# Kernel optimization log

Measured on AMD Instinct MI355X. Metric: run time of the kernel, lower is better.

Reference implementation:

```python
import jax, jax.numpy as jnp
import numpy as np

N = 100_000   # nodes
D = 64        # hidden = H * C
H, C = 8, 8   # heads, per-head channels
E = 500_000   # edges per edge set
EPS = 1e-3    # keras LayerNormalization default epsilon
RSQRT_C = np.float32(1.0 / np.sqrt(C))


def setup_inputs() -> dict:
    key = jax.random.key(0)
    ks = jax.random.split(key, 13)
    s = 0.05
    return dict(
        x=jax.random.normal(ks[0], (N, D), jnp.float32),
        src0=jax.random.randint(ks[1], (E,), 0, N, jnp.int32),
        dst0=jax.random.randint(ks[2], (E,), 0, N, jnp.int32),
        src1=jax.random.randint(ks[3], (E,), 0, N, jnp.int32),
        dst1=jax.random.randint(ks[4], (E,), 0, N, jnp.int32),
        Wk=jax.random.normal(ks[5], (D, D), jnp.float32) * s,
        bk=jnp.zeros((D,), jnp.float32),
        Wm=jax.random.normal(ks[6], (D, D), jnp.float32) * s,
        bm=jnp.zeros((D,), jnp.float32),
        Wq=jax.random.normal(ks[7], (D, D), jnp.float32) * s,
        bq=jnp.zeros((D,), jnp.float32),
        Wa=jax.random.normal(ks[8], (D, D), jnp.float32) * s,
        ba=jnp.zeros((D,), jnp.float32),
        Watt0=jax.random.normal(ks[9], (H, C, C), jnp.float32) * s,
        Wmsg0=jax.random.normal(ks[10], (H, C, C), jnp.float32) * s,
        prior0=jnp.ones((H,), jnp.float32),
        Watt1=jax.random.normal(ks[11], (H, C, C), jnp.float32) * s,
        Wmsg1=jax.random.normal(ks[12], (H, C, C), jnp.float32) * s,
        prior1=jnp.ones((H,), jnp.float32),
        skip_w=jnp.ones((1,), jnp.float32),
        ln_gamma=jnp.ones((D,), jnp.float32),
        ln_beta=jnp.zeros((D,), jnp.float32),
    )


def _edge_terms(k, m, q, src, dst, Watt, Wmsg, prior):
    # gather sender keys/messages, apply per-edge-set per-head projections
    ke = jnp.einsum('ehk,hkl->ehl', k[src], Watt)          # [E,H,C]
    score = jnp.einsum('ehc,ehc->eh', ke, q[dst]) * prior * RSQRT_C  # [E,H]
    me = jnp.einsum('ehk,hkl->ehl', m[src], Wmsg)          # [E,H,C]
    return score, me


def _forward(x, src0, dst0, src1, dst1, Wk, bk, Wm, bm, Wq, bq, Wa, ba,
             Watt0, Wmsg0, prior0, Watt1, Wmsg1, prior1,
             skip_w, ln_gamma, ln_beta):
    n = x.shape[0]
    split = lambda t: t.reshape(n, H, C)
    k = split(x @ Wk + bk)   # sender keys   [N,H,C]
    m = split(x @ Wm + bm)   # sender msgs   [N,H,C]
    q = split(x @ Wq + bq)   # receiver qrys [N,H,C]

    s0, m0 = _edge_terms(k, m, q, src0, dst0, Watt0, Wmsg0, prior0)
    s1, m1 = _edge_terms(k, m, q, src1, dst1, Watt1, Wmsg1, prior1)

    # joint segment softmax over ALL incoming edges per receiver (across edge sets)
    scores = jnp.concatenate([s0, s1], axis=0)  # [Et,H]
    msgs = jnp.concatenate([m0, m1], axis=0)    # [Et,H,C]
    recv = jnp.concatenate([dst0, dst1], axis=0)
    smax = jax.ops.segment_max(scores, recv, num_segments=n)
    ex = jnp.exp(scores - smax[recv])
    denom = jax.ops.segment_sum(ex, recv, num_segments=n)
    coef = ex / denom[recv]                      # [Et,H]

    pooled = jax.ops.segment_sum(coef[:, :, None] * msgs, recv, num_segments=n)  # [N,H,C]
    merged = pooled.reshape(n, D)
    agg = jax.nn.gelu(merged, approximate=False) @ Wa + ba
    # (dropout_rate=0.0 -> identity)
    sc = jax.nn.sigmoid(skip_w[0])               # learnable weighted skip
    out = sc * agg + (1.0 - sc) * x
    # layer norm (keras default eps=1e-3)
    mu = jnp.mean(out, axis=-1, keepdims=True)
    var = jnp.var(out, axis=-1, keepdims=True)
    return ln_gamma * (out - mu) * jax.lax.rsqrt(var + EPS) + ln_beta


def reference(x, src0, dst0, src1, dst1, Wk, bk, Wm, bm, Wq, bq, Wa, ba,
              Watt0, Wmsg0, prior0, Watt1, Wmsg1, prior1,
              skip_w, ln_gamma, ln_beta):
    return _forward(x, src0, dst0, src1, dst1, Wk, bk, Wm, bm, Wq, bq, Wa, ba,
                    Watt0, Wmsg0, prior0, Watt1, Wmsg1, prior1,
                    skip_w, ln_gamma, ln_beta)
```

## Files before the change

kernel.cpp:

```cpp
#include <hip/hip_runtime.h>
#include <hip/hip_fp16.h>
#include <cstdint>
#include <cstddef>

#define TPB 256
static constexpr float RSQRT_C_F = 0.35355339059327373f;

typedef __attribute__((ext_vector_type(8))) short bf16x8;
typedef __attribute__((ext_vector_type(4))) float f32x4;
typedef __attribute__((ext_vector_type(2))) float f32x2;

#if __has_builtin(__builtin_amdgcn_cvt_pk_f32_fp8) && __has_builtin(__builtin_amdgcn_cvt_pk_fp8_f32)
#define USE_HW_FP8 1
#endif

__device__ __forceinline__ unsigned short f2bf(float f) {
    unsigned u = __float_as_uint(f);
    u += 0x7FFFu + ((u >> 16) & 1u);
    return (unsigned short)(u >> 16);
}
__device__ __forceinline__ float bf2f(unsigned short h) {
    return __uint_as_float((unsigned)h << 16);
}
__device__ __forceinline__ float loF(unsigned u) { return __uint_as_float(u << 16); }
__device__ __forceinline__ float hiF(unsigned u) { return __uint_as_float(u); }

__device__ __forceinline__ unsigned char enc8(float v) {
#ifdef USE_HW_FP8
    return (unsigned char)(__builtin_amdgcn_cvt_pk_fp8_f32(v, v, 0, false) & 0xff);
#else
    unsigned s = (__float_as_uint(v) >> 24) & 0x80u;
    float a = fabsf(v);
    if (a < 0.015625f) {
        int m = __float2int_rn(a * 512.f);
        return (unsigned char)(s | (unsigned)m);
    }
    if (a > 448.f) return (unsigned char)(s | 0x7e);
    unsigned u = __float_as_uint(a);
    u += 0x7FFFFu + ((u >> 20) & 1u);
    unsigned e8 = ((u >> 23) & 0xffu) - 120u;
    unsigned m3 = (u >> 20) & 7u;
    if (e8 > 15u) return (unsigned char)(s | 0x7e);
    return (unsigned char)(s | (e8 << 3) | m3);
#endif
}

__device__ __forceinline__ void dec8x8(uint2 v, float* o) {
#ifdef USE_HW_FP8
    f32x2 a = __builtin_amdgcn_cvt_pk_f32_fp8((int)v.x, false);
    f32x2 b = __builtin_amdgcn_cvt_pk_f32_fp8((int)v.x, true);
    f32x2 c = __builtin_amdgcn_cvt_pk_f32_fp8((int)v.y, false);
    f32x2 d = __builtin_amdgcn_cvt_pk_f32_fp8((int)v.y, true);
    o[0] = a.x; o[1] = a.y; o[2] = b.x; o[3] = b.y;
    o[4] = c.x; o[5] = c.y; o[6] = d.x; o[7] = d.y;
#else
    unsigned w[2] = {v.x, v.y};
    #pragma unroll
    for (int i = 0; i < 8; i++) {
        unsigned bb = (w[i >> 2] >> ((i & 3) * 8)) & 0xffu;
        unsigned short hs = (unsigned short)(((bb & 0x80u) << 8) | ((bb & 0x7fu) << 7));
        __half h = *reinterpret_cast<__half*>(&hs);
        o[i] = 256.f * __half2float(h);
    }
#endif
}

__device__ __forceinline__ float wbig_elem(const float* __restrict__ Wq,
                                           const float* __restrict__ Wk,
                                           const float* __restrict__ Wm,
                                           const float* __restrict__ Watt0,
                                           const float* __restrict__ Watt1,
                                           const float* __restrict__ Wmsg0,
                                           const float* __restrict__ Wmsg1,
                                           const float* __restrict__ prior0,
                                           const float* __restrict__ prior1,
                                           int i, int col) {
    if (col < 64) return Wq[i * 64 + col];
    int j = col - 64, set = j >> 6, l = j & 63, h = l >> 3, lc = l & 7;
    const float* Win = (set < 2) ? Wk : Wm;
    const float* T = (set == 0) ? Watt0 : (set == 1) ? Watt1 : (set == 2) ? Wmsg0 : Wmsg1;
    float scale = (set == 0) ? prior0[h] * RSQRT_C_F
                : (set == 1) ? prior1[h] * RSQRT_C_F : 1.f;
    float acc = 0.f;
    #pragma unroll
    for (int c = 0; c < 8; c++) acc += Win[i * 64 + h * 8 + c] * T[h * 64 + c * 8 + lc];
    return acc * scale;
}

__global__ void setup_kernel(const float* __restrict__ Wq, const float* __restrict__ bq,
                             const float* __restrict__ Wk, const float* __restrict__ bk,
                             const float* __restrict__ Wm, const float* __restrict__ bm,
                             const float* __restrict__ Watt0, const float* __restrict__ prior0,
                             const float* __restrict__ Watt1, const float* __restrict__ prior1,
                             const float* __restrict__ Wmsg0, const float* __restrict__ Wmsg1,
                             const float* __restrict__ Wa,
                             float* __restrict__ bbig,
                             unsigned short* __restrict__ Wpack,
                             unsigned short* __restrict__ Wapack,
                             int4* __restrict__ subzero, int n4) {
    const int b = blockIdx.x, t = threadIdx.x;
    if (b < 12) {
        int p = b * TPB + t;
        if (p >= 48 * 64) return;
        bool isWa = (p >= 40 * 64);
        int pl = isWa ? p - 40 * 64 : p;
        int lane = pl & 63, ctkt = pl >> 6;
        int ct = ctkt >> 1, kt = ctkt & 1;
        int kbase = kt * 32 + (lane >> 4) * 8;
        int col = ct * 16 + (lane & 15);
        unsigned short h[8];
        if (isWa) {
            #pragma unroll
            for (int j = 0; j < 8; j++) h[j] = f2bf(Wa[(size_t)(kbase + j) * 64 + col]);
        } else {
            #pragma unroll
            for (int j = 0; j < 8; j++)
                h[j] = f2bf(wbig_elem(Wq, Wk, Wm, Watt0, Watt1, Wmsg0, Wmsg1,
                                      prior0, prior1, kbase + j, col));
        }
        uint4 pk;
        pk.x = (unsigned)h[0] | ((unsigned)h[1] << 16);
        pk.y = (unsigned)h[2] | ((unsigned)h[3] << 16);
        pk.z = (unsigned)h[4] | ((unsigned)h[5] << 16);
        pk.w = (unsigned)h[6] | ((unsigned)h[7] << 16);
        unsigned short* dst = isWa ? Wapack : Wpack;
        *(uint4*)&dst[(size_t)pl * 8] = pk;
    } else if (b < 14) {
        int col = (b - 12) * TPB + t;
        if (col >= 320) return;
        float v;
        if (col < 64) {
            v = bq[col];
        } else {
            int j = col - 64, set = j >> 6, l = j & 63, h = l >> 3, lc = l & 7;
            const float* bin = (set < 2) ? bk : bm;
            const float* T = (set == 0) ? Watt0 : (set == 1) ? Watt1 : (set == 2) ? Wmsg0 : Wmsg1;
            float scale = (set == 0) ? prior0[h] * RSQRT_C_F
                        : (set == 1) ? prior1[h] * RSQRT_C_F : 1.f;
            float acc = 0.f;
            #pragma unroll
            for (int c = 0; c < 8; c++) acc += bin[h * 8 + c] * T[h * 64 + c * 8 + lc];
            v = acc * scale;
        }
        bbig[col] = v;
    } else {
        int i = (b - 14) * TPB + t;
        int stride = 18 * TPB;
        for (; i < n4; i += stride) subzero[i] = int4{0, 0, 0, 0};
    }
}

__global__ void hist_kernel(const int* __restrict__ dst0, const int* __restrict__ dst1,
                            int* __restrict__ sub, int* __restrict__ rank,
                            int E0, int Etot, int N) {
    const int gid = blockIdx.x * TPB + threadIdx.x;
    const int S = gridDim.x * TPB;
    #pragma unroll
    for (int k = 0; k < 4; k++) {
        int e = gid + k * S;
        if (e < Etot) {
            int d = (e < E0) ? dst0[e] : dst1[e - E0];
            d = min(max(d, 0), N - 1);
            rank[e] = atomicAdd(&sub[((e >> 8) & 7) * N + d], 1);
        }
    }
}

__global__ void scan1(int* __restrict__ sub, int* __restrict__ offsets,
                      int* __restrict__ blocksums, int n) {
    __shared__ int sums[TPB];
    int b = blockIdx.x, t = threadIdx.x;
    int base = b * 1024 + t * 4;
    int cnt[4];
    #pragma unroll
    for (int i = 0; i < 4; i++) {
        int d = base + i;
        int s = 0;
        if (d < n) {
            #pragma unroll
            for (int bb = 0; bb < 8; bb++) {
                int v = sub[bb * n + d];
                sub[bb * n + d] = s;
                s += v;
            }
        }
        cnt[i] = s;
    }
    int local = cnt[0] + cnt[1] + cnt[2] + cnt[3];
    sums[t] = local;
    __syncthreads();
    for (int off = 1; off < TPB; off <<= 1) {
        int add = (t >= off) ? sums[t - off] : 0;
        __syncthreads();
        sums[t] += add;
        __syncthreads();
    }
    int excl = sums[t] - local;
    if (base + 0 < n) offsets[base + 0] = excl;
    if (base + 1 < n) offsets[base + 1] = excl + cnt[0];
    if (base + 2 < n) offsets[base + 2] = excl + cnt[0] + cnt[1];
    if (base + 3 < n) offsets[base + 3] = excl + cnt[0] + cnt[1] + cnt[2];
    if (t == TPB - 1) blocksums[b] = sums[TPB - 1];
}

__global__ void scan3(int* __restrict__ offsets, const int* __restrict__ blocksums,
                      int* __restrict__ sub, int n, int Etot, int nb) {
    __shared__ int s[TPB];
    __shared__ int excl[TPB];
    int t = threadIdx.x;
    int v = (t < nb) ? blocksums[t] : 0;
    s[t] = v;
    __syncthreads();
    for (int off = 1; off < TPB; off <<= 1) {
        int add = (t >= off) ? s[t - off] : 0;
        __syncthreads();
        s[t] += add;
        __syncthreads();
    }
    excl[t] = s[t] - v;
    __syncthreads();
    int i = blockIdx.x * TPB + t;
    if (i < n) {
        int vv = offsets[i] + excl[i >> 10];
        offsets[i] = vv;
        #pragma unroll
        for (int b = 0; b < 8; b++) sub[b * n + i] += vv;
    }
    if (i == n) offsets[n] = Etot;
}

__global__ void scatter_kernel(const int* __restrict__ src0, const int* __restrict__ dst0,
                               const int* __restrict__ src1, const int* __restrict__ dst1,
                               const int* __restrict__ sub,
                               const int* __restrict__ rank, unsigned* __restrict__ records,
                               int E0, int Etot, int N) {
    const int gid = blockIdx.x * TPB + threadIdx.x;
    const int S = gridDim.x * TPB;
    #pragma unroll
    for (int k = 0; k < 4; k++) {
        int e = gid + k * S;
        if (e < Etot) {
            int s, d, setbit;
            if (e < E0) { s = src0[e]; d = dst0[e]; setbit = 0; }
            else        { s = src1[e - E0]; d = dst1[e - E0]; setbit = 1; }
            d = min(max(d, 0), N - 1);
            int pos = sub[((e >> 8) & 7) * N + d] + rank[e];
            pos = min(max(pos, 0), Etot - 1);
            records[pos] = (unsigned)s | ((unsigned)setbit << 24);
        }
    }
}

__global__ __launch_bounds__(TPB) void proj_mfma(const float* __restrict__ x,
                                                 const unsigned short* __restrict__ Wpack,
                                                 const float* __restrict__ bbig,
                                                 unsigned short* __restrict__ qbuf,
                                                 unsigned char* __restrict__ kmbuf8,
                                                 int N) {
    const int lane = threadIdx.x & 63;
    const int wv = threadIdx.x >> 6;
    const int rb0 = blockIdx.x * 128 + wv * 16;
    const int rb1 = rb0 + 64;
    const int arow0 = min(rb0 + (lane & 15), N - 1);
    const int arow1 = min(rb1 + (lane & 15), N - 1);
    const int kbase = (lane >> 4) * 8;

    bf16x8 afA[2], afB[2];
    #pragma unroll
    for (int kt = 0; kt < 2; kt++) {
        const float* xp = x + (size_t)arow0 * 64 + kt * 32 + kbase;
        float4 v0 = *(const float4*)xp;
        float4 v1 = *(const float4*)(xp + 4);
        bf16x8 a;
        a[0] = (short)f2bf(v0.x); a[1] = (short)f2bf(v0.y);
        a[2] = (short)f2bf(v0.z); a[3] = (short)f2bf(v0.w);
        a[4] = (short)f2bf(v1.x); a[5] = (short)f2bf(v1.y);
        a[6] = (short)f2bf(v1.z); a[7] = (short)f2bf(v1.w);
        afA[kt] = a;
        const float* xq = x + (size_t)arow1 * 64 + kt * 32 + kbase;
        float4 w0 = *(const float4*)xq;
        float4 w1 = *(const float4*)(xq + 4);
        bf16x8 b;
        b[0] = (short)f2bf(w0.x); b[1] = (short)f2bf(w0.y);
        b[2] = (short)f2bf(w0.z); b[3] = (short)f2bf(w0.w);
        b[4] = (short)f2bf(w1.x); b[5] = (short)f2bf(w1.y);
        b[6] = (short)f2bf(w1.z); b[7] = (short)f2bf(w1.w);
        afB[kt] = b;
    }

    const int colq = lane & 15;
    const int rgrp = (lane >> 4) * 4;

    for (int ct = 0; ct < 20; ct++) {
        bf16x8 b0 = *(const bf16x8*)(Wpack + ((size_t)(ct * 2 + 0) * 64 + lane) * 8);
        bf16x8 b1 = *(const bf16x8*)(Wpack + ((size_t)(ct * 2 + 1) * 64 + lane) * 8);
        f32x4 accA = {0.f, 0.f, 0.f, 0.f};
        accA = __builtin_amdgcn_mfma_f32_16x16x32_bf16(afA[0], b0, accA, 0, 0, 0);
        accA = __builtin_amdgcn_mfma_f32_16x16x32_bf16(afA[1], b1, accA, 0, 0, 0);
        f32x4 accB = {0.f, 0.f, 0.f, 0.f};
        accB = __builtin_amdgcn_mfma_f32_16x16x32_bf16(afB[0], b0, accB, 0, 0, 0);
        accB = __builtin_amdgcn_mfma_f32_16x16x32_bf16(afB[1], b1, accB, 0, 0, 0);
        const int col = ct * 16 + colq;
        const float bv = bbig[col];
        if (ct < 4) {
            #pragma unroll
            for (int r = 0; r < 4; r++) {
                int row = rb0 + rgrp + r;
                if (row < N) qbuf[(size_t)row * 64 + col] = f2bf(accA[r] + bv);
                int row2 = rb1 + rgrp + r;
                if (row2 < N) qbuf[(size_t)row2 * 64 + col] = f2bf(accB[r] + bv);
            }
        } else {
            const int cm = col - 64;
            const int g = cm >> 6, w = cm & 63;
            const int addr = (g & 1) * 128 + (g >> 1) * 64 + w;
            #pragma unroll
            for (int r = 0; r < 4; r++) {
                int row = rb0 + rgrp + r;
                if (row < N) kmbuf8[(size_t)row * 256 + addr] = enc8(accA[r] + bv);
                int row2 = rb1 + rgrp + r;
                if (row2 < N) kmbuf8[(size_t)row2 * 256 + addr] = enc8(accB[r] + bv);
            }
        }
    }
}

__global__ __launch_bounds__(TPB) void pool_kernel(const unsigned short* __restrict__ qbuf,
                                                   const unsigned char* __restrict__ kmbuf8,
                                                   const unsigned* __restrict__ records,
                                                   const int* __restrict__ offsets,
                                                   unsigned short* __restrict__ pooledN,
                                                   int N) {
    const int lane = threadIdx.x & 63;
    const int j = lane & 7;
    const int r = ((blockIdx.x * TPB + threadIdx.x) >> 6) * 8 + (lane >> 3);
    if (r >= N) return;
    const int beg = offsets[r], end = offsets[r + 1];

    uint4 qv = *(const uint4*)(qbuf + (size_t)r * 64 + (j << 3));
    float qa0 = loF(qv.x), qa1 = hiF(qv.x), qa2 = loF(qv.y), qa3 = hiF(qv.y);
    float qa4 = loF(qv.z), qa5 = hiF(qv.z), qa6 = loF(qv.w), qa7 = hiF(qv.w);

    float d_run = 0.f;
    float p0 = 0.f, p1 = 0.f, p2 = 0.f, p3 = 0.f, p4 = 0.f, p5 = 0.f, p6 = 0.f, p7 = 0.f;

#define EDGE(T) {                                                              \
        unsigned rec = records[T];                                             \
        size_t base = ((size_t)(rec & 0xFFFFFFu) << 8) + (((rec >> 24) & 1u) << 7) + (j << 3); \
        uint2 kv = *(const uint2*)(kmbuf8 + base);                             \
        uint2 mv = *(const uint2*)(kmbuf8 + base + 64);                        \
        float kf[8], mf[8];                                                    \
        dec8x8(kv, kf); dec8x8(mv, mf);                                        \
        float s = kf[0] * qa0 + kf[1] * qa1 + kf[2] * qa2 + kf[3] * qa3        \
                + kf[4] * qa4 + kf[5] * qa5 + kf[6] * qa6 + kf[7] * qa7;       \
        float c = __expf(fminf(s, 60.f));                                      \
        d_run += c;                                                            \
        p0 += c * mf[0]; p1 += c * mf[1]; p2 += c * mf[2]; p3 += c * mf[3];    \
        p4 += c * mf[4]; p5 += c * mf[5]; p6 += c * mf[6]; p7 += c * mf[7];    \
    }

    int t = beg;
    for (; t + 1 < end; t += 2) { EDGE(t); EDGE(t + 1); }
    if (t < end) EDGE(t);
#undef EDGE

    const float inv = (end > beg) ? 1.f / d_run : 0.f;
    uint4 ov;
    ov.x = (unsigned)f2bf(p0 * inv) | ((unsigned)f2bf(p1 * inv) << 16);
    ov.y = (unsigned)f2bf(p2 * inv) | ((unsigned)f2bf(p3 * inv) << 16);
    ov.z = (unsigned)f2bf(p4 * inv) | ((unsigned)f2bf(p5 * inv) << 16);
    ov.w = (unsigned)f2bf(p6 * inv) | ((unsigned)f2bf(p7 * inv) << 16);
    *(uint4*)(pooledN + (size_t)r * 64 + (j << 3)) = ov;
}

__global__ __launch_bounds__(TPB) void final_mfma(const float* __restrict__ x,
                                                  const unsigned short* __restrict__ pooledN,
                                                  const unsigned short* __restrict__ Wapack,
                                                  const float* __restrict__ ba,
                                                  const float* __restrict__ skipw,
                                                  const float* __restrict__ gamma,
                                                  const float* __restrict__ beta,
                                                  float* __restrict__ out, int N) {
    const int lane = threadIdx.x & 63;
    const int wv = threadIdx.x >> 6;
    const int rowbase = blockIdx.x * 64 + wv * 16;
    const int arow = min(rowbase + (lane & 15), N - 1);
    const int kbase = (lane >> 4) * 8;
    const float sc = 1.f / (1.f + __expf(-skipw[0]));

    bf16x8 afrag[2];
    #pragma unroll
    for (int kt = 0; kt < 2; kt++) {
        uint4 pv = *(const uint4*)(pooledN + (size_t)arow * 64 + kt * 32 + kbase);
        float g[8];
        g[0] = loF(pv.x); g[1] = bf2f((unsigned short)(pv.x >> 16));
        g[2] = loF(pv.y); g[3] = bf2f((unsigned short)(pv.y >> 16));
        g[4] = loF(pv.z); g[5] = bf2f((unsigned short)(pv.z >> 16));
        g[6] = loF(pv.w); g[7] = bf2f((unsigned short)(pv.w >> 16));
        bf16x8 a;
        #pragma unroll
        for (int i = 0; i < 8; i++) {
            float gg = 0.5f * g[i] * (1.f + erff(g[i] * 0.70710678118654752f));
            a[i] = (short)f2bf(gg);
        }
        afrag[kt] = a;
    }

    const int colq = lane & 15;
    const int rgrp = (lane >> 4) * 4;

    float o[4][4];
    #pragma unroll
    for (int ct = 0; ct < 4; ct++) {
        bf16x8 b0 = *(const bf16x8*)(Wapack + ((size_t)(ct * 2 + 0) * 64 + lane) * 8);
        bf16x8 b1 = *(const bf16x8*)(Wapack + ((size_t)(ct * 2 + 1) * 64 + lane) * 8);
        f32x4 acc = {0.f, 0.f, 0.f, 0.f};
        acc = __builtin_amdgcn_mfma_f32_16x16x32_bf16(afrag[0], b0, acc, 0, 0, 0);
        acc = __builtin_amdgcn_mfma_f32_16x16x32_bf16(afrag[1], b1, acc, 0, 0, 0);
        const int col = ct * 16 + colq;
        const float bav = ba[col];
        #pragma unroll
        for (int r = 0; r < 4; r++) {
            int row = min(rowbase + rgrp + r, N - 1);
            float xv = x[(size_t)row * 64 + col];
            o[ct][r] = sc * (acc[r] + bav) + (1.f - sc) * xv;
        }
    }

    #pragma unroll
    for (int r = 0; r < 4; r++) {
        float s1 = o[0][r] + o[1][r] + o[2][r] + o[3][r];
        float s2 = o[0][r] * o[0][r] + o[1][r] * o[1][r]
                 + o[2][r] * o[2][r] + o[3][r] * o[3][r];
        #pragma unroll
        for (int off = 1; off <= 8; off <<= 1) {
            s1 += __shfl_xor(s1, off, 64);
            s2 += __shfl_xor(s2, off, 64);
        }
        float mu = s1 * (1.f / 64.f);
        float var = s2 * (1.f / 64.f) - mu * mu;
        float rs = rsqrtf(var + 1e-3f);
        const int row = rowbase + rgrp + r;
        if (row < N) {
            #pragma unroll
            for (int ct = 0; ct < 4; ct++) {
                const int col = ct * 16 + colq;
                out[(size_t)row * 64 + col] = gamma[col] * (o[ct][r] - mu) * rs + beta[col];
            }
        }
    }
}

extern "C" void kernel_launch(void* const* d_in, const int* in_sizes, int n_in,
                              void* d_out, int out_size, void* d_ws, size_t ws_size,
                              hipStream_t stream) {
    const float* x      = (const float*)d_in[0];
    const int*   src0   = (const int*)d_in[1];
    const int*   dst0   = (const int*)d_in[2];
    const int*   src1   = (const int*)d_in[3];
    const int*   dst1   = (const int*)d_in[4];
    const float* Wk     = (const float*)d_in[5];
    const float* bk     = (const float*)d_in[6];
    const float* Wm     = (const float*)d_in[7];
    const float* bm     = (const float*)d_in[8];
    const float* Wq     = (const float*)d_in[9];
    const float* bq     = (const float*)d_in[10];
    const float* Wa     = (const float*)d_in[11];
    const float* ba     = (const float*)d_in[12];
    const float* Watt0  = (const float*)d_in[13];
    const float* Wmsg0  = (const float*)d_in[14];
    const float* prior0 = (const float*)d_in[15];
    const float* Watt1  = (const float*)d_in[16];
    const float* Wmsg1  = (const float*)d_in[17];
    const float* prior1 = (const float*)d_in[18];
    const float* skipw  = (const float*)d_in[19];
    const float* gamma  = (const float*)d_in[20];
    const float* beta   = (const float*)d_in[21];

    const int N  = in_sizes[0] / 64;
    const int E0 = in_sizes[1];
    const int E1 = in_sizes[3];
    const int Etot = E0 + E1;

    float* ws       = (float*)d_ws;
    float* bbig     = ws;
    unsigned short* Wpack  = (unsigned short*)(bbig + 320);
    unsigned short* Wapack = Wpack + 40 * 64 * 8;
    unsigned short* qbuf   = Wapack + 8 * 64 * 8;
    unsigned short* pooledN = qbuf + (size_t)N * 64;
    unsigned char* kmbuf8  = (unsigned char*)(pooledN + (size_t)N * 64);
    int* sub        = (int*)(kmbuf8 + (size_t)N * 256);
    int* offsets    = sub + (size_t)8 * N;
    int* blocksums  = offsets + N + 1;
    int* rank       = blocksums + 512;
    unsigned* records = (unsigned*)(rank + Etot);

    const int nb1 = (N + 1023) / 1024;
    const int gE4 = (Etot + 4 * TPB - 1) / (4 * TPB);

    setup_kernel<<<32, TPB, 0, stream>>>(Wq, bq, Wk, bk, Wm, bm, Watt0, prior0,
                                         Watt1, prior1, Wmsg0, Wmsg1, Wa,
                                         bbig, Wpack, Wapack, (int4*)sub, 2 * N);

    proj_mfma<<<(N + 127) / 128, TPB, 0, stream>>>(x, Wpack, bbig, qbuf, kmbuf8, N);

    hist_kernel<<<gE4, TPB, 0, stream>>>(dst0, dst1, sub, rank, E0, Etot, N);

    scan1<<<nb1, TPB, 0, stream>>>(sub, offsets, blocksums, N);
    scan3<<<(N + 1 + TPB - 1) / TPB, TPB, 0, stream>>>(offsets, blocksums, sub, N, Etot, nb1);

    scatter_kernel<<<gE4, TPB, 0, stream>>>(src0, dst0, src1, dst1, sub,
                                            rank, records, E0, Etot, N);

    pool_kernel<<<((size_t)N * 8 + TPB - 1) / TPB, TPB, 0, stream>>>(qbuf, kmbuf8, records,
                                                                     offsets, pooledN, N);

    final_mfma<<<(N + 63) / 64, TPB, 0, stream>>>(x, pooledN, Wapack, ba, skipw,
                                                  gamma, beta, (float*)d_out, N);
}
```

Measured before the change: 152.8 us.

## Stage projection outputs through LDS for coalesced stores; double rows per wave in final

The projection kernel now writes per-wave MFMA results into a shared-memory tile, grouped four column tiles at a time, then stores full rows to qbuf and kmbuf8 with 16-byte vector writes. Before, it issued scattered 2-byte and 1-byte global stores. The final kernel processes two 16-row tiles per wave (128 rows per block), reusing the Wa fragments and halving the grid. This adds block-wide barriers and LDS traffic, and raises register pressure in the final kernel.

Result: faster. 145.9 us (-4.5%).

```diff
diff --git a/kernel.cpp b/kernel.cpp
--- a/kernel.cpp
+++ b/kernel.cpp
@@ -257,8 +257,10 @@
                                                  unsigned short* __restrict__ qbuf,
                                                  unsigned char* __restrict__ kmbuf8,
                                                  int N) {
+    __shared__ unsigned char ldsb[4][4096];
     const int lane = threadIdx.x & 63;
     const int wv = threadIdx.x >> 6;
+    unsigned char* L = ldsb[wv];
     const int rb0 = blockIdx.x * 128 + wv * 16;
     const int rb1 = rb0 + 64;
     const int arow0 = min(rb0 + (lane & 15), N - 1);
@@ -290,38 +292,63 @@
 
     const int colq = lane & 15;
     const int rgrp = (lane >> 4) * 4;
-
-    for (int ct = 0; ct < 20; ct++) {
-        bf16x8 b0 = *(const bf16x8*)(Wpack + ((size_t)(ct * 2 + 0) * 64 + lane) * 8);
-        bf16x8 b1 = *(const bf16x8*)(Wpack + ((size_t)(ct * 2 + 1) * 64 + lane) * 8);
-        f32x4 accA = {0.f, 0.f, 0.f, 0.f};
-        accA = __builtin_amdgcn_mfma_f32_16x16x32_bf16(afA[0], b0, accA, 0, 0, 0);
-        accA = __builtin_amdgcn_mfma_f32_16x16x32_bf16(afA[1], b1, accA, 0, 0, 0);
-        f32x4 accB = {0.f, 0.f, 0.f, 0.f};
-        accB = __builtin_amdgcn_mfma_f32_16x16x32_bf16(afB[0], b0, accB, 0, 0, 0);
-        accB = __builtin_amdgcn_mfma_f32_16x16x32_bf16(afB[1], b1, accB, 0, 0, 0);
-        const int col = ct * 16 + colq;
-        const float bv = bbig[col];
-        if (ct < 4) {
-            #pragma unroll
-            for (int r = 0; r < 4; r++) {
-                int row = rb0 + rgrp + r;
-                if (row < N) qbuf[(size_t)row * 64 + col] = f2bf(accA[r] + bv);
-                int row2 = rb1 + rgrp + r;
-                if (row2 < N) qbuf[(size_t)row2 * 64 + col] = f2bf(accB[r] + bv);
+    const int rrow = lane >> 2;
+    const int rqt = lane & 3;
+
+    for (int g = 0; g < 5; g++) {
+        #pragma unroll
+        for (int ct4 = 0; ct4 < 4; ct4++) {
+            const int ct = g * 4 + ct4;
+            bf16x8 b0 = *(const bf16x8*)(Wpack + ((size_t)(ct * 2 + 0) * 64 + lane) * 8);
+            bf16x8 b1 = *(const bf16x8*)(Wpack + ((size_t)(ct * 2 + 1) * 64 + lane) * 8);
+            f32x4 accA = {0.f, 0.f, 0.f, 0.f};
+            accA = __builtin_amdgcn_mfma_f32_16x16x32_bf16(afA[0], b0, accA, 0, 0, 0);
+            accA = __builtin_amdgcn_mfma_f32_16x16x32_bf16(afA[1], b1, accA, 0, 0, 0);
+            f32x4 accB = {0.f, 0.f, 0.f, 0.f};
+            accB = __builtin_amdgcn_mfma_f32_16x16x32_bf16(afB[0], b0, accB, 0, 0, 0);
+            accB = __builtin_amdgcn_mfma_f32_16x16x32_bf16(afB[1], b1, accB, 0, 0, 0);
+            const float bv = bbig[ct * 16 + colq];
+            const int cig = ct4 * 16 + colq;
+            if (g == 0) {
+                #pragma unroll
+                for (int r = 0; r < 4; r++) {
+                    *(unsigned short*)&L[(rgrp + r) * 128 + cig * 2]        = f2bf(accA[r] + bv);
+                    *(unsigned short*)&L[2048 + (rgrp + r) * 128 + cig * 2] = f2bf(accB[r] + bv);
+                }
+            } else {
+                #pragma unroll
+                for (int r = 0; r < 4; r++) {
+                    L[(rgrp + r) * 64 + cig]        = enc8(accA[r] + bv);
+                    L[1024 + (rgrp + r) * 64 + cig] = enc8(accB[r] + bv);
+                }
+            }
+        }
+        __syncthreads();
+        if (g == 0) {
+            #pragma unroll
+            for (int s = 0; s < 2; s++) {
+                int row = (s ? rb1 : rb0) + rrow;
+                if (row < N) {
+                    uint4 v0 = *(const uint4*)&L[s * 2048 + rrow * 128 + rqt * 32];
+                    uint4 v1 = *(const uint4*)&L[s * 2048 + rrow * 128 + rqt * 32 + 16];
+                    unsigned char* dst = (unsigned char*)qbuf + (size_t)row * 128 + rqt * 32;
+                    *(uint4*)dst = v0;
+                    *(uint4*)(dst + 16) = v1;
+                }
             }
         } else {
-            const int cm = col - 64;
-            const int g = cm >> 6, w = cm & 63;
-            const int addr = (g & 1) * 128 + (g >> 1) * 64 + w;
-            #pragma unroll
-            for (int r = 0; r < 4; r++) {
-                int row = rb0 + rgrp + r;
-                if (row < N) kmbuf8[(size_t)row * 256 + addr] = enc8(accA[r] + bv);
-                int row2 = rb1 + rgrp + r;
-                if (row2 < N) kmbuf8[(size_t)row2 * 256 + addr] = enc8(accB[r] + bv);
-            }
-        }
+            const int gg = g - 1;
+            const int gbase = (gg & 1) * 128 + (gg >> 1) * 64;
+            #pragma unroll
+            for (int s = 0; s < 2; s++) {
+                int row = (s ? rb1 : rb0) + rrow;
+                if (row < N) {
+                    uint4 v = *(const uint4*)&L[s * 1024 + rrow * 64 + rqt * 16];
+                    *(uint4*)(kmbuf8 + (size_t)row * 256 + gbase + rqt * 16) = v;
+                }
+            }
+        }
+        __syncthreads();
     }
 }
 
@@ -383,69 +410,86 @@
                                                   float* __restrict__ out, int N) {
     const int lane = threadIdx.x & 63;
     const int wv = threadIdx.x >> 6;
-    const int rowbase = blockIdx.x * 64 + wv * 16;
-    const int arow = min(rowbase + (lane & 15), N - 1);
+    const int rb0 = blockIdx.x * 128 + wv * 16;
+    const int rb1 = rb0 + 64;
+    const int arow0 = min(rb0 + (lane & 15), N - 1);
+    const int arow1 = min(rb1 + (lane & 15), N - 1);
     const int kbase = (lane >> 4) * 8;
     const float sc = 1.f / (1.f + __expf(-skipw[0]));
 
-    bf16x8 afrag[2];
+    bf16x8 afA[2], afB[2];
     #pragma unroll
     for (int kt = 0; kt < 2; kt++) {
-        uint4 pv = *(const uint4*)(pooledN + (size_t)arow * 64 + kt * 32 + kbase);
-        float g[8];
-        g[0] = loF(pv.x); g[1] = bf2f((unsigned short)(pv.x >> 16));
-        g[2] = loF(pv.y); g[3] = bf2f((unsigned short)(pv.y >> 16));
-        g[4] = loF(pv.z); g[5] = bf2f((unsigned short)(pv.z >> 16));
-        g[6] = loF(pv.w); g[7] = bf2f((unsigned short)(pv.w >> 16));
-        bf16x8 a;
         #pragma unroll
-        for (int i = 0; i < 8; i++) {
-            float gg = 0.5f * g[i] * (1.f + erff(g[i] * 0.70710678118654752f));
-            a[i] = (short)f2bf(gg);
-        }
-        afrag[kt] = a;
+        for (int s = 0; s < 2; s++) {
+            const int arow = s ? arow1 : arow0;
+            uint4 pv = *(const uint4*)(pooledN + (size_t)arow * 64 + kt * 32 + kbase);
+            float g[8];
+            g[0] = loF(pv.x); g[1] = bf2f((unsigned short)(pv.x >> 16));
+            g[2] = loF(pv.y); g[3] = bf2f((unsigned short)(pv.y >> 16));
+            g[4] = loF(pv.z); g[5] = bf2f((unsigned short)(pv.z >> 16));
+            g[6] = loF(pv.w); g[7] = bf2f((unsigned short)(pv.w >> 16));
+            bf16x8 a;
+            #pragma unroll
+            for (int i = 0; i < 8; i++) {
+                float gg = 0.5f * g[i] * (1.f + erff(g[i] * 0.70710678118654752f));
+                a[i] = (short)f2bf(gg);
+            }
+            if (s) afB[kt] = a; else afA[kt] = a;
+        }
     }
 
     const int colq = lane & 15;
     const int rgrp = (lane >> 4) * 4;
 
-    float o[4][4];
+    float oA[4][4], oB[4][4];
     #pragma unroll
     for (int ct = 0; ct < 4; ct++) {
         bf16x8 b0 = *(const bf16x8*)(Wapack + ((size_t)(ct * 2 + 0) * 64 + lane) * 8);
         bf16x8 b1 = *(const bf16x8*)(Wapack + ((size_t)(ct * 2 + 1) * 64 + lane) * 8);
-        f32x4 acc = {0.f, 0.f, 0.f, 0.f};
-        acc = __builtin_amdgcn_mfma_f32_16x16x32_bf16(afrag[0], b0, acc, 0, 0, 0);
-        acc = __builtin_amdgcn_mfma_f32_16x16x32_bf16(afrag[1], b1, acc, 0, 0, 0);
+        f32x4 accA = {0.f, 0.f, 0.f, 0.f};
+        accA = __builtin_amdgcn_mfma_f32_16x16x32_bf16(afA[0], b0, accA, 0, 0, 0);
+        accA = __builtin_amdgcn_mfma_f32_16x16x32_bf16(afA[1], b1, accA, 0, 0, 0);
+        f32x4 accB = {0.f, 0.f, 0.f, 0.f};
+        accB = __builtin_amdgcn_mfma_f32_16x16x32_bf16(afB[0], b0, accB, 0, 0, 0);
+        accB = __builtin_amdgcn_mfma_f32_16x16x32_bf16(afB[1], b1, accB, 0, 0, 0);
         const int col = ct * 16 + colq;
         const float bav = ba[col];
         #pragma unroll
         for (int r = 0; r < 4; r++) {
-            int row = min(rowbase + rgrp + r, N - 1);
-            float xv = x[(size_t)row * 64 + col];
-            o[ct][r] = sc * (acc[r] + bav) + (1.f - sc) * xv;
-        }
-    }
-
-    #pragma unroll
-    for (int r = 0; r < 4; r++) {
-        float s1 = o[0][r] + o[1][r] + o[2][r] + o[3][r];
-        float s2 = o[0][r] * o[0][r] + o[1][r] * o[1][r]
-                 + o[2][r] * o[2][r] + o[3][r] * o[3][r];
+            int rowA = min(rb0 + rgrp + r, N - 1);
+            float xvA = x[(size_t)rowA * 64 + col];
+            oA[ct][r] = sc * (accA[r] + bav) + (1.f - sc) * xvA;
+            int rowB = min(rb1 + rgrp + r, N - 1);
+            float xvB = x[(size_t)rowB * 64 + col];
+            oB[ct][r] = sc * (accB[r] + bav) + (1.f - sc) * xvB;
+        }
+    }
+
+    #pragma unroll
+    for (int s = 0; s < 2; s++) {
+        float (*o)[4] = s ? oB : oA;
+        const int rowbase = s ? rb1 : rb0;
         #pragma unroll
-        for (int off = 1; off <= 8; off <<= 1) {
-            s1 += __shfl_xor(s1, off, 64);
-            s2 += __shfl_xor(s2, off, 64);
-        }
-        float mu = s1 * (1.f / 64.f);
-        float var = s2 * (1.f / 64.f) - mu * mu;
-        float rs = rsqrtf(var + 1e-3f);
-        const int row = rowbase + rgrp + r;
-        if (row < N) {
-            #pragma unroll
-            for (int ct = 0; ct < 4; ct++) {
-                const int col = ct * 16 + colq;
-                out[(size_t)row * 64 + col] = gamma[col] * (o[ct][r] - mu) * rs + beta[col];
+        for (int r = 0; r < 4; r++) {
+            float s1 = o[0][r] + o[1][r] + o[2][r] + o[3][r];
+            float s2 = o[0][r] * o[0][r] + o[1][r] * o[1][r]
+                     + o[2][r] * o[2][r] + o[3][r] * o[3][r];
+            #pragma unroll
+            for (int off = 1; off <= 8; off <<= 1) {
+                s1 += __shfl_xor(s1, off, 64);
+                s2 += __shfl_xor(s2, off, 64);
+            }
+            float mu = s1 * (1.f / 64.f);
+            float var = s2 * (1.f / 64.f) - mu * mu;
+            float rs = rsqrtf(var + 1e-3f);
+            const int row = rowbase + rgrp + r;
+            if (row < N) {
+                #pragma unroll
+                for (int ct = 0; ct < 4; ct++) {
+                    const int col = ct * 16 + colq;
+                    out[(size_t)row * 64 + col] = gamma[col] * (o[ct][r] - mu) * rs + beta[col];
+                }
             }
         }
     }
@@ -515,6 +559,6 @@
     pool_kernel<<<((size_t)N * 8 + TPB - 1) / TPB, TPB, 0, stream>>>(qbuf, kmbuf8, records,
                                                                      offsets, pooledN, N);
 
-    final_mfma<<<(N + 63) / 64, TPB, 0, stream>>>(x, pooledN, Wapack, ba, skipw,
-                                                  gamma, beta, (float*)d_out, N);
-}
+    final_mfma<<<(N + 127) / 128, TPB, 0, stream>>>(x, pooledN, Wapack, ba, skipw,
+                                                    gamma, beta, (float*)d_out, N);
+}
```
